# Optimization experiments

Hardware: AMD Instinct MI355X
Metric: run time of the kernel (lower is better)

## Reference

```python
import jax, jax.numpy as jnp
import numpy as np

B, Hc, Wc, C, NH, SR, WS = 4, 64, 64, 256, 8, 2, 4
N = Hc * Wc


def _window_partition(x, ws, H, W):
    # x: (B, h, N, d) -> (B*h*nWin, ws*ws, d)
    Bb, h, _, d = x.shape
    x = x.reshape(Bb * h, H // ws, ws, W // ws, ws, d)
    x = x.transpose(0, 1, 3, 2, 4, 5)
    return x.reshape(-1, ws * ws, d)


def _window_reverse(win, ws, H, W, head):
    nwin = (H // ws) * (W // ws)
    Bh = win.shape[0] // nwin
    x = win.reshape(Bh, H // ws, W // ws, ws, ws, -1).transpose(0, 1, 3, 2, 4, 5).reshape(Bh, H, W, -1)
    Bb = Bh // head
    x = x.reshape(Bb, head, H, W, -1).transpose(0, 2, 3, 1, 4)  # heads interleave into channels
    return x.reshape(Bb, H * W, -1)


def _layernorm(x, w, b):
    m = x.mean(-1, keepdims=True)
    v = x.var(-1, keepdims=True)
    return (x - m) / jnp.sqrt(v + 1e-5) * w + b


def setup_inputs() -> dict:
    key = jax.random.key(0)
    ks = jax.random.split(key, 16)
    lin = lambda k, i, o: 0.02 * jax.random.normal(k, (i, o), jnp.float32)
    inp = {
        'x': jax.random.normal(ks[0], (B, N, C), jnp.float32),
        'q1_w': lin(ks[1], C, C // 2), 'q1_b': jnp.zeros((C // 2,), jnp.float32),
        'kv1_w': lin(ks[2], C, C), 'kv1_b': jnp.zeros((C,), jnp.float32),
        'q2_w': lin(ks[3], C, C // 2), 'q2_b': jnp.zeros((C // 2,), jnp.float32),
        'kv2_w': lin(ks[4], C, C), 'kv2_b': jnp.zeros((C,), jnp.float32),
        'lepe_w': lin(ks[5], C, C), 'lepe_b': jnp.zeros((C,), jnp.float32),
        'lepe_conv_w': jnp.sqrt(2.0 / 9.0) * jax.random.normal(ks[6], (C, 1, 3, 3), jnp.float32),
        'lepe_conv_b': jnp.zeros((C,), jnp.float32),
        'sr_w': jnp.sqrt(2.0 / (SR * SR * C)) * jax.random.normal(ks[7], (C, C, SR, SR), jnp.float32),
        'sr_b': jnp.zeros((C,), jnp.float32),
        'norm_w': jnp.ones((C,), jnp.float32), 'norm_b': jnp.zeros((C,), jnp.float32),
        'proj_w': lin(ks[8], C, C), 'proj_b': jnp.zeros((C,), jnp.float32),
        'H': Hc, 'W': Wc,
    }
    return inp


def reference(x, q1_w, q1_b, kv1_w, kv1_b, q2_w, q2_b, kv2_w, kv2_b,
              lepe_w, lepe_b, lepe_conv_w, lepe_conv_b, sr_w, sr_b,
              norm_w, norm_b, proj_w, proj_b, H, W):
    Bb, Nn, Cc = x.shape
    h2 = NH // 2
    d = Cc // NH
    sr = sr_w.shape[-1]
    scale = d ** -0.5
    ws = WS

    # lepe: linear -> depthwise 3x3 conv
    l = (x @ lepe_w + lepe_b).transpose(0, 2, 1).reshape(Bb, Cc, H, W)
    l = jax.lax.conv_general_dilated(l, lepe_conv_w, (1, 1), ((1, 1), (1, 1)),
                                     dimension_numbers=('NCHW', 'OIHW', 'NCHW'),
                                     feature_group_count=Cc) + lepe_conv_b[None, :, None, None]
    lepe = l.reshape(Bb, Cc, Nn).transpose(0, 2, 1)

    # branch 1: spatial-reduction global attention
    q1 = (x @ q1_w + q1_b).reshape(Bb, Nn, h2, d).transpose(0, 2, 1, 3)
    x_img = x.transpose(0, 2, 1).reshape(Bb, Cc, H, W)
    xs = jax.lax.conv_general_dilated(x_img, sr_w, (sr, sr), 'VALID',
                                      dimension_numbers=('NCHW', 'OIHW', 'NCHW')) + sr_b[None, :, None, None]
    N1 = (H // sr) * (W // sr)
    xs = xs.reshape(Bb, Cc, N1).transpose(0, 2, 1)
    xs = jax.nn.gelu(_layernorm(xs, norm_w, norm_b), approximate=False)
    kv1 = (xs @ kv1_w + kv1_b).reshape(Bb, N1, 2, h2, d).transpose(2, 0, 3, 1, 4)
    k1, v1 = kv1[0], kv1[1]
    attn1 = jax.nn.softmax(jnp.einsum('bhnd,bhmd->bhnm', q1, k1) * scale, axis=-1)
    x1 = jnp.einsum('bhnm,bhmd->bnhd', attn1, v1).reshape(Bb, Nn, Cc // 2)
    g = jax.lax.stop_gradient(attn1).mean(1).mean(1).reshape(Bb, H // sr, W // sr)
    g = jnp.repeat(jnp.repeat(g, sr, axis=1), sr, axis=2)  # nearest upsample to (B,H,W)

    # branch 2: Swin-style windowed attention (window 4)
    q2 = (x @ q2_w + q2_b).reshape(Bb, Nn, h2, d).transpose(0, 2, 1, 3)
    kv2 = (x @ kv2_w + kv2_b).reshape(Bb, Nn, 2, h2, d).transpose(2, 0, 3, 1, 4)
    k2, v2 = kv2[0], kv2[1]
    q2w = _window_partition(q2, ws, H, W)
    k2w = _window_partition(k2, ws, H, W)
    v2w = _window_partition(v2, ws, H, W)
    attn2 = jax.nn.softmax(jnp.einsum('wnd,wmd->wnm', q2w, k2w) * scale, axis=-1)
    x2 = jnp.einsum('wnm,wmd->wnd', attn2, v2w)
    x2 = _window_reverse(x2, ws, H, W, h2)
    nwin = (H // ws) * (W // ws)
    lm = jax.lax.stop_gradient(attn2).reshape(Bb, h2, nwin, ws * ws, ws * ws).mean(1).mean(2)
    lm = lm.reshape(Bb, H // ws, W // ws, ws, ws).transpose(0, 1, 3, 2, 4).reshape(Bb, H, W)

    out = jnp.concatenate([x1, x2], axis=-1)
    p = (out + lepe) @ proj_w + proj_b
    out = p + p  # proj_drop is identity at p=0.0, so x = drop(p) + p = 2p

    mask = lm + g
    mask1 = mask.reshape(Bb, H * W)
    mask2 = mask.transpose(0, 2, 1).reshape(Bb, H * W)
    return out, mask1, mask2
```

## Files before the change

kernel.cpp:

```cpp
#include <hip/hip_runtime.h>
#include <hip/hip_bf16.h>
#include <math.h>

typedef __hip_bfloat16 bf16;
typedef __attribute__((ext_vector_type(8))) short bf16x8;
typedef __attribute__((ext_vector_type(4))) short bf16x4;
typedef __attribute__((ext_vector_type(4))) float f32x4;

__device__ __forceinline__ float b2f(bf16 v) { return __bfloat162float(v); }
__device__ __forceinline__ bf16  f2b(float v) { return __float2bfloat16(v); }
__device__ __forceinline__ float s2f(short v) { return __uint_as_float(((unsigned)(unsigned short)v) << 16); }

__global__ void detect_dtype(const void* x, int* flag)
{
    __shared__ int cnt;
    if (threadIdx.x == 0) cnt = 0;
    __syncthreads();
    const unsigned* w = (const unsigned*)x;
    int sane = 0;
    for (int i = threadIdx.x; i < 2048; i += 256) {
        unsigned lo = (w[i] & 0xFFFFu) << 16;
        float v = __uint_as_float(lo);
        float a = fabsf(v);
        if (v == 0.f || (a > 1e-8f && a < 1e4f)) sane++;
    }
    atomicAdd(&cnt, sane);
    __syncthreads();
    if (threadIdx.x == 0) *flag = (cnt < 1640) ? 1 : 0;
}

__global__ void convert_x4(const void* __restrict__ src, bf16* __restrict__ dst,
                           const int* __restrict__ flag)
{
    int i = blockIdx.x * 256 + threadIdx.x;
    bf16 tmp[4];
    if (*flag) {
        float4 v = ((const float4*)src)[i];
        tmp[0] = f2b(v.x); tmp[1] = f2b(v.y); tmp[2] = f2b(v.z); tmp[3] = f2b(v.w);
        *(bf16x4*)&dst[i * 4] = *(bf16x4*)tmp;
    } else {
        ((bf16x4*)dst)[i] = ((const bf16x4*)src)[i];
    }
}

struct PackArgs { const void* src[10]; bf16* dst[10]; int n[10]; };
__global__ void pack_small(PackArgs a, const int* __restrict__ flag)
{
    int bi = blockIdx.x;
    int n = a.n[bi];
    const void* s = a.src[bi];
    bf16* d = a.dst[bi];
    for (int i = threadIdx.x; i < n; i += 256)
        d[i] = (*flag) ? f2b(((const float*)s)[i]) : f2b(s2f(((const short*)s)[i]));
}

struct WTArgs { const void* src[6]; bf16* dst[6]; int N[6]; int blkoff[7]; };
__global__ void convert_wT_multi(WTArgs a, const int* __restrict__ flag)
{
    int blk = blockIdx.x;
    int ti = 0;
    while (blk >= a.blkoff[ti + 1]) ++ti;
    int o = (blk - a.blkoff[ti]) * 256 + threadIdx.x;
    int n = o >> 8, k = o & 255;
    int N = a.N[ti];
    float v = (*flag) ? ((const float*)a.src[ti])[k * N + n]
                      : s2f(((const short*)a.src[ti])[k * N + n]);
    a.dst[ti][o] = f2b(v);
}

__global__ void convert_srwT(const void* __restrict__ src, bf16* __restrict__ dst,
                             const int* __restrict__ flag)
{
    int o = blockIdx.x * 256 + threadIdx.x;
    int co = o >> 10, kg = o & 1023;
    int e = kg >> 8, ci = kg & 255;
    int si = co * 1024 + ci * 4 + e;
    float v = (*flag) ? ((const float*)src)[si] : s2f(((const short*)src)[si]);
    dst[o] = f2b(v);
}

__global__ void convert_dwT(const void* __restrict__ src, bf16* __restrict__ dst,
                            const int* __restrict__ flag)
{
    int o = blockIdx.x * 256 + threadIdx.x;
    if (o >= 2304) return;
    int k = o >> 8, c = o & 255;
    float v = (*flag) ? ((const float*)src)[c * 9 + k] : s2f(((const short*)src)[c * 9 + k]);
    dst[o] = f2b(v);
}

__global__ __launch_bounds__(256) void gemm_qkv128(
    const bf16* __restrict__ A, const bf16* __restrict__ WT, const bf16* __restrict__ bias,
    bf16* __restrict__ Cl, bf16* __restrict__ Cq1, bf16* __restrict__ Cq2, bf16* __restrict__ Ckv2)
{
    __shared__ bf16 As[128][40];
    __shared__ bf16 Bs[128][40];
    int t = threadIdx.x;
    int m0 = blockIdx.x * 128, ybase = blockIdx.y * 128;
    int w = t >> 6, l = t & 63, lane16 = l & 15, quad = l >> 4;
    int wr = w >> 1, wc = w & 1;
    int sr = t >> 1, sc = (t & 1) * 16;
    f32x4 acc[4][4] = {};
    for (int k0 = 0; k0 < 256; k0 += 32) {
        *(bf16x8*)&As[sr][sc]     = *(const bf16x8*)&A[(size_t)(m0 + sr) * 256 + k0 + sc];
        *(bf16x8*)&As[sr][sc + 8] = *(const bf16x8*)&A[(size_t)(m0 + sr) * 256 + k0 + sc + 8];
        *(bf16x8*)&Bs[sr][sc]     = *(const bf16x8*)&WT[(size_t)(ybase + sr) * 256 + k0 + sc];
        *(bf16x8*)&Bs[sr][sc + 8] = *(const bf16x8*)&WT[(size_t)(ybase + sr) * 256 + k0 + sc + 8];
        __syncthreads();
        bf16x8 a[4], b[4];
        #pragma unroll
        for (int i = 0; i < 4; ++i) {
            a[i] = *(const bf16x8*)&As[wr * 64 + i * 16 + lane16][quad * 8];
            b[i] = *(const bf16x8*)&Bs[wc * 64 + i * 16 + lane16][quad * 8];
        }
        #pragma unroll
        for (int i = 0; i < 4; ++i)
            #pragma unroll
            for (int j = 0; j < 4; ++j)
                acc[i][j] = __builtin_amdgcn_mfma_f32_16x16x32_bf16(a[i], b[j], acc[i][j], 0, 0, 0);
        __syncthreads();
    }
    bf16* C; int N, cbase;
    if (ybase < 256)      { C = Cl;   N = 256; cbase = ybase; }
    else if (ybase < 384) { C = Cq1;  N = 128; cbase = ybase - 256; }
    else if (ybase < 512) { C = Cq2;  N = 128; cbase = ybase - 384; }
    else                  { C = Ckv2; N = 256; cbase = ybase - 512; }
    #pragma unroll
    for (int j = 0; j < 4; ++j) {
        int gcol = ybase + wc * 64 + j * 16 + lane16;
        float bv = b2f(bias[gcol]);
        int col = cbase + wc * 64 + j * 16 + lane16;
        #pragma unroll
        for (int i = 0; i < 4; ++i)
            #pragma unroll
            for (int r = 0; r < 4; ++r) {
                int row = m0 + wr * 64 + i * 16 + quad * 4 + r;
                C[(size_t)row * N + col] = f2b(acc[i][j][r] + bv);
            }
    }
}

__global__ __launch_bounds__(256) void gemm_proj128(
    const bf16* __restrict__ A, const bf16* __restrict__ A2,
    const bf16* __restrict__ WT, const bf16* __restrict__ bias,
    void* __restrict__ dout, const int* __restrict__ flag)
{
    __shared__ bf16 As[128][40];
    __shared__ bf16 Bs[128][40];
    int t = threadIdx.x;
    int m0 = blockIdx.x * 128, n0 = blockIdx.y * 128;
    int w = t >> 6, l = t & 63, lane16 = l & 15, quad = l >> 4;
    int wr = w >> 1, wc = w & 1;
    int sr = t >> 1, sc = (t & 1) * 16;
    f32x4 acc[4][4] = {};
    for (int k0 = 0; k0 < 256; k0 += 32) {
        #pragma unroll
        for (int hh = 0; hh < 2; ++hh) {
            bf16x8 va = *(const bf16x8*)&A[(size_t)(m0 + sr) * 256 + k0 + sc + hh * 8];
            bf16x8 vb = *(const bf16x8*)&A2[(size_t)(m0 + sr) * 256 + k0 + sc + hh * 8];
            bf16 tmp[8];
            #pragma unroll
            for (int q = 0; q < 8; ++q) tmp[q] = f2b(s2f(va[q]) + s2f(vb[q]));
            *(bf16x8*)&As[sr][sc + hh * 8] = *(bf16x8*)tmp;
        }
        *(bf16x8*)&Bs[sr][sc]     = *(const bf16x8*)&WT[(size_t)(n0 + sr) * 256 + k0 + sc];
        *(bf16x8*)&Bs[sr][sc + 8] = *(const bf16x8*)&WT[(size_t)(n0 + sr) * 256 + k0 + sc + 8];
        __syncthreads();
        bf16x8 a[4], b[4];
        #pragma unroll
        for (int i = 0; i < 4; ++i) {
            a[i] = *(const bf16x8*)&As[wr * 64 + i * 16 + lane16][quad * 8];
            b[i] = *(const bf16x8*)&Bs[wc * 64 + i * 16 + lane16][quad * 8];
        }
        #pragma unroll
        for (int i = 0; i < 4; ++i)
            #pragma unroll
            for (int j = 0; j < 4; ++j)
                acc[i][j] = __builtin_amdgcn_mfma_f32_16x16x32_bf16(a[i], b[j], acc[i][j], 0, 0, 0);
        __syncthreads();
    }
    #pragma unroll
    for (int j = 0; j < 4; ++j) {
        int col = n0 + wc * 64 + j * 16 + lane16;
        float bv = b2f(bias[col]);
        #pragma unroll
        for (int i = 0; i < 4; ++i)
            #pragma unroll
            for (int r = 0; r < 4; ++r) {
                int row = m0 + wr * 64 + i * 16 + quad * 4 + r;
                float rv = (acc[i][j][r] + bv) * 2.f;
                size_t o = (size_t)row * 256 + col;
                if (*flag) ((float*)dout)[o] = rv;
                else       ((bf16*)dout)[o] = f2b(rv);
            }
    }
}

__global__ __launch_bounds__(256) void gemm_sr_mfma(
    const bf16* __restrict__ x, const bf16* __restrict__ WT,
    const bf16* __restrict__ bias, bf16* __restrict__ C)
{
    __shared__ bf16 As[64][40];
    __shared__ bf16 Bs[64][40];
    int t = threadIdx.x;
    int m0 = blockIdx.x * 64, n0 = blockIdx.y * 64;
    int w = t >> 6, l = t & 63, lane16 = l & 15, quad = l >> 4;
    int sr = t >> 2, sc = (t & 3) * 8;
    int brow = m0 + sr;
    int b = brow >> 10, p = brow & 1023;
    int pi = p >> 5, pj = p & 31;
    f32x4 acc[4] = {};
    for (int k0 = 0; k0 < 1024; k0 += 32) {
        int kg = k0 + sc;
        int e = kg >> 8, ci = kg & 255;
        int di = e >> 1, dj = e & 1;
        int n = (2 * pi + di) * 64 + 2 * pj + dj;
        *(bf16x8*)&As[sr][sc] = *(const bf16x8*)&x[(size_t)((b << 12) + n) * 256 + ci];
        *(bf16x8*)&Bs[sr][sc] = *(const bf16x8*)&WT[(size_t)(n0 + sr) * 1024 + kg];
        __syncthreads();
        bf16x8 a = *(const bf16x8*)&As[w * 16 + lane16][quad * 8];
        #pragma unroll
        for (int ct = 0; ct < 4; ++ct) {
            bf16x8 bb = *(const bf16x8*)&Bs[ct * 16 + lane16][quad * 8];
            acc[ct] = __builtin_amdgcn_mfma_f32_16x16x32_bf16(a, bb, acc[ct], 0, 0, 0);
        }
        __syncthreads();
    }
    #pragma unroll
    for (int ct = 0; ct < 4; ++ct) {
        int col = n0 + ct * 16 + lane16;
        float bv = b2f(bias[col]);
        #pragma unroll
        for (int r = 0; r < 4; ++r) {
            int row = m0 + w * 16 + quad * 4 + r;
            C[(size_t)row * 256 + col] = f2b(acc[ct][r] + bv);
        }
    }
}

__global__ __launch_bounds__(256) void gemm_kv1(
    const bf16* __restrict__ A, const bf16* __restrict__ WT, const bf16* __restrict__ bias,
    bf16* __restrict__ k1, bf16* __restrict__ v1T)
{
    __shared__ bf16 As[64][40];
    __shared__ bf16 Bs[64][40];
    int t = threadIdx.x;
    int m0 = blockIdx.x * 64, n0 = blockIdx.y * 64;
    int w = t >> 6, l = t & 63, lane16 = l & 15, quad = l >> 4;
    int sr = t >> 2, sc = (t & 3) * 8;
    f32x4 acc[4] = {};
    for (int k0 = 0; k0 < 256; k0 += 32) {
        *(bf16x8*)&As[sr][sc] = *(const bf16x8*)&A[(size_t)(m0 + sr) * 256 + k0 + sc];
        *(bf16x8*)&Bs[sr][sc] = *(const bf16x8*)&WT[(size_t)(n0 + sr) * 256 + k0 + sc];
        __syncthreads();
        bf16x8 a = *(const bf16x8*)&As[w * 16 + lane16][quad * 8];
        #pragma unroll
        for (int ct = 0; ct < 4; ++ct) {
            bf16x8 b = *(const bf16x8*)&Bs[ct * 16 + lane16][quad * 8];
            acc[ct] = __builtin_amdgcn_mfma_f32_16x16x32_bf16(a, b, acc[ct], 0, 0, 0);
        }
        __syncthreads();
    }
    #pragma unroll
    for (int ct = 0; ct < 4; ++ct) {
        int col = n0 + ct * 16 + lane16;
        float bv = b2f(bias[col]);
        #pragma unroll
        for (int r = 0; r < 4; ++r) {
            int row = m0 + w * 16 + quad * 4 + r;
            float val = acc[ct][r] + bv;
            int bb = row >> 10, key = row & 1023;
            if (col < 128) {
                k1[(size_t)row * 128 + col] = f2b(val);
            } else {
                int h = (col - 128) >> 5, ch = (col - 128) & 31;
                v1T[(size_t)((bb * 4 + h) * 32 + ch) * 1024 + key] = f2b(val);
            }
        }
    }
}

__global__ __launch_bounds__(256) void dwconv3v(
    const bf16* __restrict__ lin, const bf16* __restrict__ dwT,
    const bf16* __restrict__ bias, bf16* __restrict__ out)
{
    int tid = blockIdx.x * 256 + threadIdx.x;
    int c0 = (tid & 31) * 8;
    int n = (tid >> 5) & 4095;
    int b = tid >> 17;
    int i = n >> 6, j = n & 63;
    float acc[8];
    bf16x8 bv = *(const bf16x8*)&bias[c0];
    #pragma unroll
    for (int q = 0; q < 8; ++q) acc[q] = s2f(bv[q]);
    #pragma unroll
    for (int di = 0; di < 3; ++di) {
        int ii = i + di - 1;
        if (ii < 0 || ii > 63) continue;
        #pragma unroll
        for (int dj = 0; dj < 3; ++dj) {
            int jj = j + dj - 1;
            if (jj < 0 || jj > 63) continue;
            bf16x8 xv = *(const bf16x8*)&lin[(size_t)((b << 12) + ii * 64 + jj) * 256 + c0];
            bf16x8 wv = *(const bf16x8*)&dwT[(di * 3 + dj) * 256 + c0];
            #pragma unroll
            for (int q = 0; q < 8; ++q) acc[q] += s2f(xv[q]) * s2f(wv[q]);
        }
    }
    bf16 ov[8];
    #pragma unroll
    for (int q = 0; q < 8; ++q) ov[q] = f2b(acc[q]);
    *(bf16x8*)&out[(size_t)((b << 12) + n) * 256 + c0] = *(bf16x8*)ov;
}

__global__ __launch_bounds__(256) void ln_gelu_w(
    const bf16* __restrict__ xin, const bf16* __restrict__ nw,
    const bf16* __restrict__ nb, bf16* __restrict__ xout)
{
    int w = threadIdx.x >> 6, lane = threadIdx.x & 63;
    int r = blockIdx.x * 4 + w;
    bf16x4 xv = *(const bf16x4*)&xin[(size_t)r * 256 + lane * 4];
    float v[4];
    #pragma unroll
    for (int j = 0; j < 4; ++j) v[j] = s2f(xv[j]);
    float s = v[0] + v[1] + v[2] + v[3];
    #pragma unroll
    for (int o = 1; o <= 32; o <<= 1) s += __shfl_xor(s, o);
    float mean = s * (1.f / 256.f);
    float ss = 0.f;
    #pragma unroll
    for (int j = 0; j < 4; ++j) { float d = v[j] - mean; ss += d * d; }
    #pragma unroll
    for (int o = 1; o <= 32; o <<= 1) ss += __shfl_xor(ss, o);
    float inv = rsqrtf(ss * (1.f / 256.f) + 1e-5f);
    bf16x4 wv = *(const bf16x4*)&nw[lane * 4];
    bf16x4 bv = *(const bf16x4*)&nb[lane * 4];
    bf16 ov[4];
    #pragma unroll
    for (int j = 0; j < 4; ++j) {
        float y = (v[j] - mean) * inv * s2f(wv[j]) + s2f(bv[j]);
        ov[j] = f2b(0.5f * y * (1.f + erff(y * 0.70710678118654752f)));
    }
    *(bf16x4*)&xout[(size_t)r * 256 + lane * 4] = *(bf16x4*)ov;
}

__global__ __launch_bounds__(512) void attn1_split(
    const bf16* __restrict__ q1, const bf16* __restrict__ k1,
    const bf16* __restrict__ v1T, bf16* __restrict__ attn_out, float* __restrict__ g)
{
    __shared__ bf16 Kt[2][64][40];
    __shared__ bf16 Vt[2][32][68];
    __shared__ bf16 PTT[8][16][72];
    __shared__ float gp[1024];
    __shared__ float Lcmb[4][16];
    __shared__ float rls[4][16];
    __shared__ __align__(16) float Ocmb[4][16][36];

    int t = threadIdx.x;
    int blk = blockIdx.x;
    int qc = blk & 63, h = (blk >> 6) & 3, b = blk >> 8;
    int n0 = qc * 64;
    int w = t >> 6, l = t & 63, lane16 = l & 15, quad = l >> 4;
    int grp = w >> 2, qg = w & 3;
    int tg = t & 255;
    const float scale = 0.17677669529663687f;

    const bf16* Kbase = k1 + (size_t)b * 1024 * 128 + 32 * h + (size_t)(grp * 512) * 128;
    const bf16* Vbase = v1T + (size_t)((b * 4 + h) * 32) * 1024 + grp * 512;
    bf16x8 qa = *(const bf16x8*)&q1[(size_t)(b * 4096 + n0 + 16 * qg + lane16) * 128 + 32 * h + quad * 8];

    for (int i = t; i < 1024; i += 512) gp[i] = 0.f;

    int sr = tg >> 2, sc = (tg & 3) * 8;
    int vrow = tg >> 3, vcol = (tg & 7) * 8;
    bf16* ptt = &PTT[w][0][0];

    float lacc = 0.f;
    f32x4 oT0 = {}, oT1 = {};

    for (int ktl = 0; ktl < 8; ++ktl) {
        *(bf16x8*)&Kt[grp][sr][sc] = *(const bf16x8*)&Kbase[(size_t)(ktl * 64 + sr) * 128 + sc];
        *(bf16x8*)&Vt[grp][vrow][vcol] = *(const bf16x8*)&Vbase[(size_t)vrow * 1024 + ktl * 64 + vcol];
        __syncthreads();
        #pragma unroll
        for (int st = 0; st < 4; ++st) {
            bf16x8 kf = *(const bf16x8*)&Kt[grp][st * 16 + lane16][quad * 8];
            f32x4 z = {0.f, 0.f, 0.f, 0.f};
            f32x4 sT = __builtin_amdgcn_mfma_f32_16x16x32_bf16(kf, qa, z, 0, 0, 0);
            bf16 pk[4];
            #pragma unroll
            for (int r = 0; r < 4; ++r) {
                float p = __expf(sT[r] * scale);
                lacc += p;
                pk[r] = f2b(p);
            }
            *(bf16x4*)&ptt[lane16 * 72 + st * 16 + quad * 4] = *(bf16x4*)pk;
        }
        #pragma unroll
        for (int kh = 0; kh < 2; ++kh) {
            bf16x8 pf = *(const bf16x8*)&ptt[lane16 * 72 + kh * 32 + quad * 8];
            bf16x8 vf0 = *(const bf16x8*)&Vt[grp][lane16][kh * 32 + quad * 8];
            bf16x8 vf1 = *(const bf16x8*)&Vt[grp][16 + lane16][kh * 32 + quad * 8];
            oT0 = __builtin_amdgcn_mfma_f32_16x16x32_bf16(vf0, pf, oT0, 0, 0, 0);
            oT1 = __builtin_amdgcn_mfma_f32_16x16x32_bf16(vf1, pf, oT1, 0, 0, 0);
        }
        __syncthreads();
    }

    lacc += __shfl_xor(lacc, 16);
    lacc += __shfl_xor(lacc, 32);

    if (grp == 1) {
        if (quad == 0) Lcmb[qg][lane16] = lacc;
        *(f32x4*)&Ocmb[qg][lane16][quad * 4]      = oT0;
        *(f32x4*)&Ocmb[qg][lane16][16 + quad * 4] = oT1;
    }
    __syncthreads();
    if (grp == 0) {
        float ltot = lacc + Lcmb[qg][lane16];
        float rl = 1.f / ltot;
        if (quad == 0) rls[qg][lane16] = rl;
        f32x4 p0 = *(const f32x4*)&Ocmb[qg][lane16][quad * 4];
        f32x4 p1 = *(const f32x4*)&Ocmb[qg][lane16][16 + quad * 4];
        bf16 ov0[4], ov1[4];
        #pragma unroll
        for (int r = 0; r < 4; ++r) {
            ov0[r] = f2b((oT0[r] + p0[r]) * rl);
            ov1[r] = f2b((oT1[r] + p1[r]) * rl);
        }
        size_t ro = (size_t)(b * 4096 + n0 + 16 * qg + lane16) * 256 + 32 * h;
        *(bf16x4*)&attn_out[ro + quad * 4]      = *(bf16x4*)ov0;
        *(bf16x4*)&attn_out[ro + 16 + quad * 4] = *(bf16x4*)ov1;
    }
    __syncthreads();

    float rlq[4];
    #pragma unroll
    for (int r = 0; r < 4; ++r) rlq[r] = rls[qg][quad * 4 + r];

    int sr2 = tg >> 2, sc2 = (tg & 3) * 8;
    for (int ktl = 0; ktl < 8; ++ktl) {
        *(bf16x8*)&Kt[grp][sr2][sc2] = *(const bf16x8*)&Kbase[(size_t)(ktl * 64 + sr2) * 128 + sc2];
        __syncthreads();
        #pragma unroll
        for (int st = 0; st < 4; ++st) {
            bf16x8 kf = *(const bf16x8*)&Kt[grp][st * 16 + lane16][quad * 8];
            f32x4 z = {0.f, 0.f, 0.f, 0.f};
            f32x4 s = __builtin_amdgcn_mfma_f32_16x16x32_bf16(qa, kf, z, 0, 0, 0);
            float cs = 0.f;
            #pragma unroll
            for (int r = 0; r < 4; ++r) cs += __expf(s[r] * scale) * rlq[r];
            cs += __shfl_xor(cs, 16);
            cs += __shfl_xor(cs, 32);
            if (quad == 0) atomicAdd(&gp[grp * 512 + ktl * 64 + st * 16 + lane16], cs);
        }
        __syncthreads();
    }

    for (int i = t; i < 1024; i += 512)
        atomicAdd(&g[(b << 10) + i], gp[i] * (1.f / 16384.f));
}

__global__ __launch_bounds__(64) void attn2_vec(
    const bf16* __restrict__ q2, const bf16* __restrict__ kv2,
    bf16* __restrict__ attn_out, float* __restrict__ lm)
{
    __shared__ float P2[64][17];
    int t = threadIdx.x;
    int blk = blockIdx.x;
    int b = blk >> 8, win = blk & 255;
    int wi = win >> 4, wj = win & 15;
    int h = t >> 4, qi = t & 15;
    int nq = (wi * 4 + (qi >> 2)) * 64 + wj * 4 + (qi & 3);

    float qv[32];
    {
        const bf16* qp = q2 + (size_t)(b * 4096 + nq) * 128 + h * 32;
        #pragma unroll
        for (int g8 = 0; g8 < 4; ++g8) {
            bf16x8 v = *(const bf16x8*)&qp[g8 * 8];
            #pragma unroll
            for (int j = 0; j < 8; ++j) qv[g8 * 8 + j] = s2f(v[j]) * 0.17677669529663687f;
        }
    }
    float s[16];
    float mx = -1e30f;
    #pragma unroll
    for (int k = 0; k < 16; ++k) {
        int nk = (wi * 4 + (k >> 2)) * 64 + wj * 4 + (k & 3);
        const bf16* kp = kv2 + (size_t)(b * 4096 + nk) * 256 + h * 32;
        float ss = 0.f;
        #pragma unroll
        for (int g8 = 0; g8 < 4; ++g8) {
            bf16x8 v = *(const bf16x8*)&kp[g8 * 8];
            #pragma unroll
            for (int j = 0; j < 8; ++j) ss += qv[g8 * 8 + j] * s2f(v[j]);
        }
        s[k] = ss;
        mx = fmaxf(mx, ss);
    }
    float lsum = 0.f;
    #pragma unroll
    for (int k = 0; k < 16; ++k) { s[k] = __expf(s[k] - mx); lsum += s[k]; }
    float rl = 1.f / lsum;
    #pragma unroll
    for (int k = 0; k < 16; ++k) s[k] *= rl;

    float o[32];
    #pragma unroll
    for (int d = 0; d < 32; ++d) o[d] = 0.f;
    #pragma unroll
    for (int k = 0; k < 16; ++k) {
        int nk = (wi * 4 + (k >> 2)) * 64 + wj * 4 + (k & 3);
        const bf16* vp = kv2 + (size_t)(b * 4096 + nk) * 256 + 128 + h * 32;
        float p = s[k];
        #pragma unroll
        for (int g8 = 0; g8 < 4; ++g8) {
            bf16x8 v = *(const bf16x8*)&vp[g8 * 8];
            #pragma unroll
            for (int j = 0; j < 8; ++j) o[g8 * 8 + j] += p * s2f(v[j]);
        }
    }
    {
        bf16* op = attn_out + (size_t)(b * 4096 + nq) * 256 + 128 + h * 32;
        #pragma unroll
        for (int g8 = 0; g8 < 4; ++g8) {
            bf16 ov[8];
            #pragma unroll
            for (int j = 0; j < 8; ++j) ov[j] = f2b(o[g8 * 8 + j]);
            *(bf16x8*)&op[g8 * 8] = *(bf16x8*)ov;
        }
    }

    #pragma unroll
    for (int k = 0; k < 16; ++k) P2[t][k] = s[k];
    __syncthreads();
    if (t < 16) {
        float cs = 0.f;
        for (int qq = 0; qq < 64; ++qq) cs += P2[qq][t];
        int nk = (wi * 4 + (t >> 2)) * 64 + wj * 4 + (t & 3);
        lm[(b << 12) + nk] = cs * (1.f / 64.f);
    }
}

__global__ void mask_combine(const float* __restrict__ lm, const float* __restrict__ g,
                             void* __restrict__ dout, const int* __restrict__ flag)
{
    int tid = blockIdx.x * 256 + threadIdx.x;
    int b = tid >> 12, n = tid & 4095;
    int i = n >> 6, j = n & 63;
    float v = lm[tid] + g[(b << 10) + (i >> 1) * 32 + (j >> 1)];
    size_t o1 = (size_t)4194304 + (b << 12) + i * 64 + j;
    size_t o2 = (size_t)4194304 + 16384 + (b << 12) + j * 64 + i;
    if (*flag) { ((float*)dout)[o1] = v; ((float*)dout)[o2] = v; }
    else       { ((bf16*)dout)[o1] = f2b(v); ((bf16*)dout)[o2] = f2b(v); }
}

extern "C" void kernel_launch(void* const* d_in, const int* in_sizes, int n_in,
                              void* d_out, int out_size, void* d_ws, size_t ws_size,
                              hipStream_t stream)
{
    char* ws = (char*)d_ws;
    size_t off = 0;
    auto alloc = [&](size_t bytes) {
        void* p = ws + off;
        off += (bytes + 255) & ~(size_t)255;
        return p;
    };
    bf16* cx       = (bf16*)alloc((size_t)4194304 * 2);
    bf16* lepe_lin = (bf16*)alloc((size_t)4194304 * 2);
    bf16* attn_out = lepe_lin;
    bf16* lepe     = (bf16*)alloc((size_t)4194304 * 2);
    bf16* q1buf    = (bf16*)alloc((size_t)2097152 * 2);
    bf16* q2buf    = (bf16*)alloc((size_t)2097152 * 2);
    bf16* kv2buf   = (bf16*)alloc((size_t)4194304 * 2);
    bf16* xs_pre   = (bf16*)alloc((size_t)1048576 * 2);
    bf16* k1buf    = xs_pre;
    bf16* v1Tbuf   = xs_pre + 524288;
    bf16* xs       = (bf16*)alloc((size_t)1048576 * 2);
    bf16* wTqkv    = (bf16*)alloc((size_t)196608 * 2);
    bf16* kv1_wT   = (bf16*)alloc(65536 * 2);
    bf16* proj_wT  = (bf16*)alloc(65536 * 2);
    bf16* sr_wT    = (bf16*)alloc(262144 * 2);
    bf16* dwT      = (bf16*)alloc(2304 * 2);
    bf16* bcat     = (bf16*)alloc(768 * 2);
    bf16* ckv1b    = (bf16*)alloc(256 * 2);
    bf16* csrb     = (bf16*)alloc(256 * 2);
    bf16* cnw      = (bf16*)alloc(256 * 2);
    bf16* cnb      = (bf16*)alloc(256 * 2);
    bf16* cpb      = (bf16*)alloc(256 * 2);
    bf16* clcb     = (bf16*)alloc(256 * 2);
    float* gbuf    = (float*)alloc(4096 * 4);
    float* lmbuf   = (float*)alloc(16384 * 4);
    int*   flag    = (int*)alloc(256);

    detect_dtype<<<1, 256, 0, stream>>>(d_in[0], flag);

    convert_x4<<<4096, 256, 0, stream>>>(d_in[0], cx, flag);

    PackArgs pa;
    pa.src[0] = d_in[10]; pa.dst[0] = bcat;       pa.n[0] = 256;
    pa.src[1] = d_in[2];  pa.dst[1] = bcat + 256; pa.n[1] = 128;
    pa.src[2] = d_in[6];  pa.dst[2] = bcat + 384; pa.n[2] = 128;
    pa.src[3] = d_in[8];  pa.dst[3] = bcat + 512; pa.n[3] = 256;
    pa.src[4] = d_in[4];  pa.dst[4] = ckv1b;      pa.n[4] = 256;
    pa.src[5] = d_in[14]; pa.dst[5] = csrb;       pa.n[5] = 256;
    pa.src[6] = d_in[15]; pa.dst[6] = cnw;        pa.n[6] = 256;
    pa.src[7] = d_in[16]; pa.dst[7] = cnb;        pa.n[7] = 256;
    pa.src[8] = d_in[18]; pa.dst[8] = cpb;        pa.n[8] = 256;
    pa.src[9] = d_in[12]; pa.dst[9] = clcb;       pa.n[9] = 256;
    pack_small<<<10, 256, 0, stream>>>(pa, flag);

    WTArgs wa;
    wa.src[0] = d_in[9];  wa.dst[0] = wTqkv;             wa.N[0] = 256;
    wa.src[1] = d_in[1];  wa.dst[1] = wTqkv + 256 * 256; wa.N[1] = 128;
    wa.src[2] = d_in[5];  wa.dst[2] = wTqkv + 384 * 256; wa.N[2] = 128;
    wa.src[3] = d_in[7];  wa.dst[3] = wTqkv + 512 * 256; wa.N[3] = 256;
    wa.src[4] = d_in[3];  wa.dst[4] = kv1_wT;            wa.N[4] = 256;
    wa.src[5] = d_in[17]; wa.dst[5] = proj_wT;           wa.N[5] = 256;
    int bo[7] = {0, 256, 384, 512, 768, 1024, 1280};
    for (int i = 0; i < 7; ++i) wa.blkoff[i] = bo[i];
    convert_wT_multi<<<1280, 256, 0, stream>>>(wa, flag);

    convert_srwT<<<1024, 256, 0, stream>>>(d_in[13], sr_wT, flag);
    convert_dwT<<<9, 256, 0, stream>>>(d_in[11], dwT, flag);

    hipMemsetAsync(gbuf, 0, 4096 * 4, stream);

    gemm_qkv128<<<dim3(128, 6), 256, 0, stream>>>(cx, wTqkv, bcat, lepe_lin, q1buf, q2buf, kv2buf);
    gemm_sr_mfma<<<dim3(64, 4), 256, 0, stream>>>(cx, sr_wT, csrb, xs_pre);
    ln_gelu_w<<<1024, 256, 0, stream>>>(xs_pre, cnw, cnb, xs);
    gemm_kv1<<<dim3(64, 4), 256, 0, stream>>>(xs, kv1_wT, ckv1b, k1buf, v1Tbuf);
    dwconv3v<<<2048, 256, 0, stream>>>(lepe_lin, dwT, clcb, lepe);
    attn1_split<<<1024, 512, 0, stream>>>(q1buf, k1buf, v1Tbuf, attn_out, gbuf);
    attn2_vec<<<1024, 64, 0, stream>>>(q2buf, kv2buf, attn_out, lmbuf);
    gemm_proj128<<<dim3(128, 2), 256, 0, stream>>>(attn_out, lepe, proj_wT, cpb, d_out, flag);
    mask_combine<<<64, 256, 0, stream>>>(lmbuf, gbuf, d_out, flag);
}
```

Baseline: 268.3 us.

## Use MFMA for window attention, pair rows in dwconv, merge convert kernels

Rewrites the windowed-attention kernel so each wavefront handles one head with bf16 MFMA for QK^T and PV, replacing per-thread scalar dot products, and accumulates mask column sums through shared-memory atomics. The depthwise conv now computes two output rows per thread with the weights held in registers, so neighbouring input rows are reused. The attn1 mask loop reads K directly from global memory instead of staging it in LDS, which removes two barriers per tile. Three small weight-conversion kernels become one launch. The costs are bf16 rounding of the probabilities before the PV MFMA and uncached global reads for K.

```diff
diff --git a/kernel.cpp b/kernel.cpp
--- a/kernel.cpp
+++ b/kernel.cpp
@@ -43,15 +43,36 @@
     }
 }
 
-struct PackArgs { const void* src[10]; bf16* dst[10]; int n[10]; };
-__global__ void pack_small(PackArgs a, const int* __restrict__ flag)
-{
-    int bi = blockIdx.x;
-    int n = a.n[bi];
-    const void* s = a.src[bi];
-    bf16* d = a.dst[bi];
-    for (int i = threadIdx.x; i < n; i += 256)
-        d[i] = (*flag) ? f2b(((const float*)s)[i]) : f2b(s2f(((const short*)s)[i]));
+struct MiscArgs {
+    const void* srw;  bf16* srwT;
+    const void* dww;  bf16* dwT;
+    const void* psrc[10]; bf16* pdst[10]; int pn[10];
+};
+__global__ void convert_misc(MiscArgs a, const int* __restrict__ flag)
+{
+    int blk = blockIdx.x, t = threadIdx.x;
+    int fl = *flag;
+    if (blk < 1024) {
+        int o = blk * 256 + t;
+        int co = o >> 10, kg = o & 1023;
+        int e = kg >> 8, ci = kg & 255;
+        int si = co * 1024 + ci * 4 + e;
+        float v = fl ? ((const float*)a.srw)[si] : s2f(((const short*)a.srw)[si]);
+        a.srwT[o] = f2b(v);
+    } else if (blk < 1033) {
+        int o = (blk - 1024) * 256 + t;
+        if (o >= 2304) return;
+        int k = o >> 8, c = o & 255;
+        float v = fl ? ((const float*)a.dww)[c * 9 + k] : s2f(((const short*)a.dww)[c * 9 + k]);
+        a.dwT[o] = f2b(v);
+    } else {
+        int bi = blk - 1033;
+        int n = a.pn[bi];
+        const void* s = a.psrc[bi];
+        bf16* d = a.pdst[bi];
+        for (int i = t; i < n; i += 256)
+            d[i] = fl ? f2b(((const float*)s)[i]) : f2b(s2f(((const short*)s)[i]));
+    }
 }
 
 struct WTArgs { const void* src[6]; bf16* dst[6]; int N[6]; int blkoff[7]; };
@@ -66,27 +87,6 @@
     float v = (*flag) ? ((const float*)a.src[ti])[k * N + n]
                       : s2f(((const short*)a.src[ti])[k * N + n]);
     a.dst[ti][o] = f2b(v);
-}
-
-__global__ void convert_srwT(const void* __restrict__ src, bf16* __restrict__ dst,
-                             const int* __restrict__ flag)
-{
-    int o = blockIdx.x * 256 + threadIdx.x;
-    int co = o >> 10, kg = o & 1023;
-    int e = kg >> 8, ci = kg & 255;
-    int si = co * 1024 + ci * 4 + e;
-    float v = (*flag) ? ((const float*)src)[si] : s2f(((const short*)src)[si]);
-    dst[o] = f2b(v);
-}
-
-__global__ void convert_dwT(const void* __restrict__ src, bf16* __restrict__ dst,
-                            const int* __restrict__ flag)
-{
-    int o = blockIdx.x * 256 + threadIdx.x;
-    if (o >= 2304) return;
-    int k = o >> 8, c = o & 255;
-    float v = (*flag) ? ((const float*)src)[c * 9 + k] : s2f(((const short*)src)[c * 9 + k]);
-    dst[o] = f2b(v);
 }
 
 __global__ __launch_bounds__(256) void gemm_qkv128(
@@ -280,37 +280,53 @@
     }
 }
 
-__global__ __launch_bounds__(256) void dwconv3v(
+__global__ __launch_bounds__(256) void dwconv3p(
     const bf16* __restrict__ lin, const bf16* __restrict__ dwT,
     const bf16* __restrict__ bias, bf16* __restrict__ out)
 {
     int tid = blockIdx.x * 256 + threadIdx.x;
     int c0 = (tid & 31) * 8;
-    int n = (tid >> 5) & 4095;
-    int b = tid >> 17;
-    int i = n >> 6, j = n & 63;
-    float acc[8];
+    int j  = (tid >> 5) & 63;
+    int i  = ((tid >> 11) & 31) * 2;
+    int b  = tid >> 16;
+    float acc0[8], acc1[8];
     bf16x8 bv = *(const bf16x8*)&bias[c0];
     #pragma unroll
-    for (int q = 0; q < 8; ++q) acc[q] = s2f(bv[q]);
-    #pragma unroll
-    for (int di = 0; di < 3; ++di) {
-        int ii = i + di - 1;
+    for (int q = 0; q < 8; ++q) { acc0[q] = s2f(bv[q]); acc1[q] = s2f(bv[q]); }
+    bf16x8 wv[3][3];
+    #pragma unroll
+    for (int di = 0; di < 3; ++di)
+        #pragma unroll
+        for (int dj = 0; dj < 3; ++dj)
+            wv[di][dj] = *(const bf16x8*)&dwT[(di * 3 + dj) * 256 + c0];
+    #pragma unroll
+    for (int r = -1; r <= 2; ++r) {
+        int ii = i + r;
         if (ii < 0 || ii > 63) continue;
         #pragma unroll
         for (int dj = 0; dj < 3; ++dj) {
             int jj = j + dj - 1;
             if (jj < 0 || jj > 63) continue;
             bf16x8 xv = *(const bf16x8*)&lin[(size_t)((b << 12) + ii * 64 + jj) * 256 + c0];
-            bf16x8 wv = *(const bf16x8*)&dwT[(di * 3 + dj) * 256 + c0];
-            #pragma unroll
-            for (int q = 0; q < 8; ++q) acc[q] += s2f(xv[q]) * s2f(wv[q]);
+            if (r <= 1) {
+                bf16x8 w0 = wv[r + 1][dj];
+                #pragma unroll
+                for (int q = 0; q < 8; ++q) acc0[q] += s2f(xv[q]) * s2f(w0[q]);
+            }
+            if (r >= 0) {
+                bf16x8 w1 = wv[r][dj];
+                #pragma unroll
+                for (int q = 0; q < 8; ++q) acc1[q] += s2f(xv[q]) * s2f(w1[q]);
+            }
         }
     }
     bf16 ov[8];
     #pragma unroll
-    for (int q = 0; q < 8; ++q) ov[q] = f2b(acc[q]);
-    *(bf16x8*)&out[(size_t)((b << 12) + n) * 256 + c0] = *(bf16x8*)ov;
+    for (int q = 0; q < 8; ++q) ov[q] = f2b(acc0[q]);
+    *(bf16x8*)&out[(size_t)((b << 12) + i * 64 + j) * 256 + c0] = *(bf16x8*)ov;
+    #pragma unroll
+    for (int q = 0; q < 8; ++q) ov[q] = f2b(acc1[q]);
+    *(bf16x8*)&out[(size_t)((b << 12) + (i + 1) * 64 + j) * 256 + c0] = *(bf16x8*)ov;
 }
 
 __global__ __launch_bounds__(256) void ln_gelu_w(
@@ -438,13 +454,10 @@
     #pragma unroll
     for (int r = 0; r < 4; ++r) rlq[r] = rls[qg][quad * 4 + r];
 
-    int sr2 = tg >> 2, sc2 = (tg & 3) * 8;
     for (int ktl = 0; ktl < 8; ++ktl) {
-        *(bf16x8*)&Kt[grp][sr2][sc2] = *(const bf16x8*)&Kbase[(size_t)(ktl * 64 + sr2) * 128 + sc2];
-        __syncthreads();
         #pragma unroll
         for (int st = 0; st < 4; ++st) {
-            bf16x8 kf = *(const bf16x8*)&Kt[grp][st * 16 + lane16][quad * 8];
+            bf16x8 kf = *(const bf16x8*)&Kbase[(size_t)(ktl * 64 + st * 16 + lane16) * 128 + quad * 8];
             f32x4 z = {0.f, 0.f, 0.f, 0.f};
             f32x4 s = __builtin_amdgcn_mfma_f32_16x16x32_bf16(qa, kf, z, 0, 0, 0);
             float cs = 0.f;
@@ -454,92 +467,96 @@
             cs += __shfl_xor(cs, 32);
             if (quad == 0) atomicAdd(&gp[grp * 512 + ktl * 64 + st * 16 + lane16], cs);
         }
-        __syncthreads();
-    }
+    }
+    __syncthreads();
 
     for (int i = t; i < 1024; i += 512)
         atomicAdd(&g[(b << 10) + i], gp[i] * (1.f / 16384.f));
 }
 
-__global__ __launch_bounds__(64) void attn2_vec(
+__global__ __launch_bounds__(256) void attn2_mfma(
     const bf16* __restrict__ q2, const bf16* __restrict__ kv2,
     bf16* __restrict__ attn_out, float* __restrict__ lm)
 {
-    __shared__ float P2[64][17];
+    __shared__ bf16 PT2[4][16 * 40];
+    __shared__ float lmw[16];
     int t = threadIdx.x;
     int blk = blockIdx.x;
     int b = blk >> 8, win = blk & 255;
     int wi = win >> 4, wj = win & 15;
-    int h = t >> 4, qi = t & 15;
-    int nq = (wi * 4 + (qi >> 2)) * 64 + wj * 4 + (qi & 3);
-
-    float qv[32];
+    int h = t >> 6, l = t & 63, lane16 = l & 15, quad = l >> 4;
+    const float scale = 0.17677669529663687f;
+
+    if (t < 16) lmw[t] = 0.f;
+    bf16* ptt = &PT2[h][0];
     {
-        const bf16* qp = q2 + (size_t)(b * 4096 + nq) * 128 + h * 32;
-        #pragma unroll
-        for (int g8 = 0; g8 < 4; ++g8) {
-            bf16x8 v = *(const bf16x8*)&qp[g8 * 8];
-            #pragma unroll
-            for (int j = 0; j < 8; ++j) qv[g8 * 8 + j] = s2f(v[j]) * 0.17677669529663687f;
-        }
-    }
-    float s[16];
-    float mx = -1e30f;
-    #pragma unroll
-    for (int k = 0; k < 16; ++k) {
-        int nk = (wi * 4 + (k >> 2)) * 64 + wj * 4 + (k & 3);
-        const bf16* kp = kv2 + (size_t)(b * 4096 + nk) * 256 + h * 32;
-        float ss = 0.f;
-        #pragma unroll
-        for (int g8 = 0; g8 < 4; ++g8) {
-            bf16x8 v = *(const bf16x8*)&kp[g8 * 8];
-            #pragma unroll
-            for (int j = 0; j < 8; ++j) ss += qv[g8 * 8 + j] * s2f(v[j]);
-        }
-        s[k] = ss;
-        mx = fmaxf(mx, ss);
-    }
-    float lsum = 0.f;
-    #pragma unroll
-    for (int k = 0; k < 16; ++k) { s[k] = __expf(s[k] - mx); lsum += s[k]; }
+        bf16 zz[4] = {};
+        *(bf16x4*)&ptt[lane16 * 40 + 16 + quad * 4] = *(bf16x4*)zz;
+    }
+    __syncthreads();
+
+    size_t base = (size_t)(b * 4096);
+    int r0 = wi * 4, c0w = wj * 4;
+    int tq = (r0 + (lane16 >> 2)) * 64 + c0w + (lane16 & 3);
+
+    bf16x8 qa = *(const bf16x8*)&q2[(base + tq) * 128 + h * 32 + quad * 8];
+    bf16x8 kf = *(const bf16x8*)&kv2[(base + tq) * 256 + h * 32 + quad * 8];
+
+    f32x4 z = {0.f, 0.f, 0.f, 0.f};
+    f32x4 sT = __builtin_amdgcn_mfma_f32_16x16x32_bf16(kf, qa, z, 0, 0, 0);
+    float sv[4];
+    #pragma unroll
+    for (int r = 0; r < 4; ++r) sv[r] = sT[r] * scale;
+    float mx = fmaxf(fmaxf(sv[0], sv[1]), fmaxf(sv[2], sv[3]));
+    mx = fmaxf(mx, __shfl_xor(mx, 16));
+    mx = fmaxf(mx, __shfl_xor(mx, 32));
+    float p[4], lsum = 0.f;
+    #pragma unroll
+    for (int r = 0; r < 4; ++r) { p[r] = __expf(sv[r] - mx); lsum += p[r]; }
+    lsum += __shfl_xor(lsum, 16);
+    lsum += __shfl_xor(lsum, 32);
     float rl = 1.f / lsum;
-    #pragma unroll
-    for (int k = 0; k < 16; ++k) s[k] *= rl;
-
-    float o[32];
-    #pragma unroll
-    for (int d = 0; d < 32; ++d) o[d] = 0.f;
-    #pragma unroll
-    for (int k = 0; k < 16; ++k) {
-        int nk = (wi * 4 + (k >> 2)) * 64 + wj * 4 + (k & 3);
-        const bf16* vp = kv2 + (size_t)(b * 4096 + nk) * 256 + 128 + h * 32;
-        float p = s[k];
-        #pragma unroll
-        for (int g8 = 0; g8 < 4; ++g8) {
-            bf16x8 v = *(const bf16x8*)&vp[g8 * 8];
-            #pragma unroll
-            for (int j = 0; j < 8; ++j) o[g8 * 8 + j] += p * s2f(v[j]);
-        }
-    }
+    bf16 pk[4];
+    #pragma unroll
+    for (int r = 0; r < 4; ++r) { p[r] *= rl; pk[r] = f2b(p[r]); }
+    *(bf16x4*)&ptt[lane16 * 40 + quad * 4] = *(bf16x4*)pk;
+
+    bf16x8 vf0 = {}, vf1 = {};
+    if (quad < 2) {
+        #pragma unroll
+        for (int jj = 0; jj < 8; ++jj) {
+            int key = quad * 8 + jj;
+            int tk = (r0 + (key >> 2)) * 64 + c0w + (key & 3);
+            const short* vp = (const short*)&kv2[(base + tk) * 256 + 128 + h * 32];
+            vf0[jj] = vp[lane16];
+            vf1[jj] = vp[16 + lane16];
+        }
+    }
+    bf16x8 pf = *(const bf16x8*)&ptt[lane16 * 40 + quad * 8];
+    f32x4 o0 = __builtin_amdgcn_mfma_f32_16x16x32_bf16(vf0, pf, z, 0, 0, 0);
+    f32x4 o1 = __builtin_amdgcn_mfma_f32_16x16x32_bf16(vf1, pf, z, 0, 0, 0);
     {
-        bf16* op = attn_out + (size_t)(b * 4096 + nq) * 256 + 128 + h * 32;
-        #pragma unroll
-        for (int g8 = 0; g8 < 4; ++g8) {
-            bf16 ov[8];
-            #pragma unroll
-            for (int j = 0; j < 8; ++j) ov[j] = f2b(o[g8 * 8 + j]);
-            *(bf16x8*)&op[g8 * 8] = *(bf16x8*)ov;
-        }
-    }
-
-    #pragma unroll
-    for (int k = 0; k < 16; ++k) P2[t][k] = s[k];
+        bf16 ov0[4], ov1[4];
+        #pragma unroll
+        for (int r = 0; r < 4; ++r) { ov0[r] = f2b(o0[r]); ov1[r] = f2b(o1[r]); }
+        bf16* op = attn_out + (base + tq) * 256 + 128 + h * 32;
+        *(bf16x4*)&op[quad * 4]      = *(bf16x4*)ov0;
+        *(bf16x4*)&op[16 + quad * 4] = *(bf16x4*)ov1;
+    }
+
+    #pragma unroll
+    for (int r = 0; r < 4; ++r) {
+        float c = p[r];
+        c += __shfl_xor(c, 1);
+        c += __shfl_xor(c, 2);
+        c += __shfl_xor(c, 4);
+        c += __shfl_xor(c, 8);
+        if (lane16 == 0) atomicAdd(&lmw[quad * 4 + r], c);
+    }
     __syncthreads();
     if (t < 16) {
-        float cs = 0.f;
-        for (int qq = 0; qq < 64; ++qq) cs += P2[qq][t];
-        int nk = (wi * 4 + (t >> 2)) * 64 + wj * 4 + (t & 3);
-        lm[(b << 12) + nk] = cs * (1.f / 64.f);
+        int nk = (r0 + (t >> 2)) * 64 + c0w + (t & 3);
+        lm[(b << 12) + nk] = lmw[t] * (1.f / 64.f);
     }
 }
 
@@ -598,18 +615,20 @@
 
     convert_x4<<<4096, 256, 0, stream>>>(d_in[0], cx, flag);
 
-    PackArgs pa;
-    pa.src[0] = d_in[10]; pa.dst[0] = bcat;       pa.n[0] = 256;
-    pa.src[1] = d_in[2];  pa.dst[1] = bcat + 256; pa.n[1] = 128;
-    pa.src[2] = d_in[6];  pa.dst[2] = bcat + 384; pa.n[2] = 128;
-    pa.src[3] = d_in[8];  pa.dst[3] = bcat + 512; pa.n[3] = 256;
-    pa.src[4] = d_in[4];  pa.dst[4] = ckv1b;      pa.n[4] = 256;
-    pa.src[5] = d_in[14]; pa.dst[5] = csrb;       pa.n[5] = 256;
-    pa.src[6] = d_in[15]; pa.dst[6] = cnw;        pa.n[6] = 256;
-    pa.src[7] = d_in[16]; pa.dst[7] = cnb;        pa.n[7] = 256;
-    pa.src[8] = d_in[18]; pa.dst[8] = cpb;        pa.n[8] = 256;
-    pa.src[9] = d_in[12]; pa.dst[9] = clcb;       pa.n[9] = 256;
-    pack_small<<<10, 256, 0, stream>>>(pa, flag);
+    MiscArgs ma;
+    ma.srw = d_in[13]; ma.srwT = sr_wT;
+    ma.dww = d_in[11]; ma.dwT = dwT;
+    ma.psrc[0] = d_in[10]; ma.pdst[0] = bcat;       ma.pn[0] = 256;
+    ma.psrc[1] = d_in[2];  ma.pdst[1] = bcat + 256; ma.pn[1] = 128;
+    ma.psrc[2] = d_in[6];  ma.pdst[2] = bcat + 384; ma.pn[2] = 128;
+    ma.psrc[3] = d_in[8];  ma.pdst[3] = bcat + 512; ma.pn[3] = 256;
+    ma.psrc[4] = d_in[4];  ma.pdst[4] = ckv1b;      ma.pn[4] = 256;
+    ma.psrc[5] = d_in[14]; ma.pdst[5] = csrb;       ma.pn[5] = 256;
+    ma.psrc[6] = d_in[15]; ma.pdst[6] = cnw;        ma.pn[6] = 256;
+    ma.psrc[7] = d_in[16]; ma.pdst[7] = cnb;        ma.pn[7] = 256;
+    ma.psrc[8] = d_in[18]; ma.pdst[8] = cpb;        ma.pn[8] = 256;
+    ma.psrc[9] = d_in[12]; ma.pdst[9] = clcb;       ma.pn[9] = 256;
+    convert_misc<<<1043, 256, 0, stream>>>(ma, flag);
 
     WTArgs wa;
     wa.src[0] = d_in[9];  wa.dst[0] = wTqkv;             wa.N[0] = 256;
@@ -622,18 +641,15 @@
     for (int i = 0; i < 7; ++i) wa.blkoff[i] = bo[i];
     convert_wT_multi<<<1280, 256, 0, stream>>>(wa, flag);
 
-    convert_srwT<<<1024, 256, 0, stream>>>(d_in[13], sr_wT, flag);
-    convert_dwT<<<9, 256, 0, stream>>>(d_in[11], dwT, flag);
-
     hipMemsetAsync(gbuf, 0, 4096 * 4, stream);
 
     gemm_qkv128<<<dim3(128, 6), 256, 0, stream>>>(cx, wTqkv, bcat, lepe_lin, q1buf, q2buf, kv2buf);
     gemm_sr_mfma<<<dim3(64, 4), 256, 0, stream>>>(cx, sr_wT, csrb, xs_pre);
     ln_gelu_w<<<1024, 256, 0, stream>>>(xs_pre, cnw, cnb, xs);
     gemm_kv1<<<dim3(64, 4), 256, 0, stream>>>(xs, kv1_wT, ckv1b, k1buf, v1Tbuf);
-    dwconv3v<<<2048, 256, 0, stream>>>(lepe_lin, dwT, clcb, lepe);
+    dwconv3p<<<1024, 256, 0, stream>>>(lepe_lin, dwT, clcb, lepe);
     attn1_split<<<1024, 512, 0, stream>>>(q1buf, k1buf, v1Tbuf, attn_out, gbuf);
-    attn2_vec<<<1024, 64, 0, stream>>>(q2buf, kv2buf, attn_out, lmbuf);
+    attn2_mfma<<<1024, 256, 0, stream>>>(q2buf, kv2buf, attn_out, lmbuf);
     gemm_proj128<<<dim3(128, 2), 256, 0, stream>>>(attn_out, lepe, proj_wT, cpb, d_out, flag);
     mask_combine<<<64, 256, 0, stream>>>(lmbuf, gbuf, d_out, flag);
 }
```

New measurement: 254.0 us. 5.3% less time.
